# Optimization experiments

Hardware: AMD Instinct MI355X
Metric: run time of the kernel (lower is better)

## Reference

```python
import jax, jax.numpy as jnp
import numpy as np

DELTA_V = 0.5
DELTA_D = 1.5
ALPHA = 1.0
BETA = 1.0
GAMMA = 0.001
K = 32          # max number of instance labels per image
EPS = 1e-12     # sqrt safety for masked/degenerate distances


def setup_inputs() -> dict:
    key = jax.random.key(0)
    k1, k2 = jax.random.split(key)
    B, F, H, W = 8, 32, 512, 512
    embeds = jax.random.normal(k1, (B, F, H, W), dtype=jnp.float32)
    labels = jax.random.randint(k2, (B, 1, H, W), 0, K, dtype=jnp.int32)
    return {"embeds": embeds, "labels": labels}


def _disc_loss(embeds, labels):
    B, F, H, W = embeds.shape
    N = H * W
    x = embeds.reshape(B, F, N)                     # [B,F,N]
    lab = labels.reshape(B, N)                      # [B,N]

    oh = jax.nn.one_hot(lab, K, dtype=x.dtype)      # [B,N,K]
    counts = oh.sum(axis=1)                         # [B,K] pixels per label
    present = counts > 0                            # [B,K]
    pres_f = present.astype(x.dtype)
    C = pres_f.sum(axis=-1)                         # [B] number of instances
    safe_counts = jnp.maximum(counts, 1.0)

    # per-label means (fused segment reduction as one GEMM)
    sums = jnp.einsum('bfn,bnk->bfk', x, oh)        # [B,F,K]
    mu = sums / safe_counts[:, None, :]             # [B,F,K]

    # --- variance (pull) term ---
    mu_pix = jnp.einsum('bfk,bnk->bfn', mu, oh)     # mean broadcast back to pixels
    d = jnp.sqrt(jnp.sum((mu_pix - x) ** 2, axis=1) + EPS)   # [B,N] ||mu_c - x||
    v = jnp.maximum(d - DELTA_V, 0.0) ** 2
    v_per = jnp.einsum('bn,bnk->bk', v, oh) / safe_counts    # per-label mean
    var_b = jnp.where(C > 0, (v_per * pres_f).sum(-1) / jnp.maximum(C, 1.0), 0.0)
    var_loss = var_b.sum()

    # --- distance (push) term: pairwise between cluster means ---
    diff = mu[:, :, :, None] - mu[:, :, None, :]    # [B,F,K,K]
    dist = jnp.sqrt(jnp.sum(diff ** 2, axis=1) + EPS)        # [B,K,K]
    pair = present[:, :, None] & present[:, None, :]
    upper = jnp.triu(jnp.ones((K, K), dtype=bool), k=1)      # ca < cb pairs
    pm = pair & upper[None]
    hinge = jnp.maximum(DELTA_D - dist, 0.0) ** 2
    dloss = jnp.where(pm, hinge, 0.0).sum(axis=(-1, -2))     # [B]
    denom = jnp.maximum(C * (C - 1.0), 1.0)
    dis_loss = jnp.where(C > 2, dloss / denom, 0.0).sum()

    # --- regularization term: sum of ||mu_c|| over present labels ---
    mu_norm = jnp.sqrt(jnp.sum(mu ** 2, axis=1) + EPS)       # [B,K]
    reg_b = jnp.where(C > 1, (mu_norm * pres_f).sum(-1), 0.0)
    reg_loss = reg_b.sum()

    return ALPHA * var_loss + BETA * dis_loss + GAMMA * reg_loss


def reference(embeds, labels):
    return _disc_loss(embeds, labels)
```

## Files before the change

### kernel.cpp

```cpp
#include <hip/hip_runtime.h>

#define KLAB 32
#define FDIM 32
#define NPIX (512 * 512)
#define BATCH 8
#define EPSF 1e-12f

typedef __attribute__((ext_vector_type(8))) short bf16x8;
typedef __attribute__((ext_vector_type(4))) short bf16x4;
typedef __attribute__((ext_vector_type(4))) float f32x4;

__device__ __forceinline__ short f2bf(float f) {
    unsigned u = __builtin_bit_cast(unsigned, f);
    unsigned r = (u + 0x7FFFu + ((u >> 16) & 1u)) >> 16;
    return (short)r;
}

__device__ __forceinline__ float bf2f(short s) {
    return __builtin_bit_cast(float, (unsigned)((unsigned short)s) << 16);
}

__global__ __launch_bounds__(256) void k_msums(
    const float* __restrict__ x, const int* __restrict__ lab,
    float* __restrict__ g_sums, float* __restrict__ g_cnt,
    short* __restrict__ xbf)
{
    const int tid = threadIdx.x;
    const int b = blockIdx.y;
    const int w = tid >> 6, l = tid & 63;
    const int row = l & 15, grp = l >> 4;
    const int gw = blockIdx.x * 4 + w;
    const int STEPS = NPIX / 32 / 1024;
    const size_t xb = (size_t)b * FDIM * NPIX;
    const size_t lb = (size_t)b * NPIX;

    f32x4 acc00{}, acc01{}, acc10{}, acc11{}, accC0{}, accC1{};
    bf16x8 ones;
#pragma unroll
    for (int j = 0; j < 8; ++j) ones[j] = (short)0x3F80;

    const float* xr0 = x + xb + (size_t)row * NPIX;
    const float* xr1 = x + xb + (size_t)(row + 16) * NPIX;
    short* sr0 = xbf + xb + (size_t)row * NPIX;
    short* sr1 = xbf + xb + (size_t)(row + 16) * NPIX;

    int pg = gw * STEPS * 32 + grp * 8;
    int4 la = *reinterpret_cast<const int4*>(&lab[lb + pg]);
    int4 lc = *reinterpret_cast<const int4*>(&lab[lb + pg + 4]);
    f32x4 v0 = *reinterpret_cast<const f32x4*>(&xr0[pg]);
    f32x4 v1 = *reinterpret_cast<const f32x4*>(&xr0[pg + 4]);
    f32x4 v2 = *reinterpret_cast<const f32x4*>(&xr1[pg]);
    f32x4 v3 = *reinterpret_cast<const f32x4*>(&xr1[pg + 4]);

#pragma unroll 1
    for (int s = 0; s < STEPS; ++s) {
        const int pgn = pg + 32;
        int4 lan{}, lcn{};
        f32x4 w0{}, w1{}, w2{}, w3{};
        if (s + 1 < STEPS) {
            lan = *reinterpret_cast<const int4*>(&lab[lb + pgn]);
            lcn = *reinterpret_cast<const int4*>(&lab[lb + pgn + 4]);
            w0 = *reinterpret_cast<const f32x4*>(&xr0[pgn]);
            w1 = *reinterpret_cast<const f32x4*>(&xr0[pgn + 4]);
            w2 = *reinterpret_cast<const f32x4*>(&xr1[pgn]);
            w3 = *reinterpret_cast<const f32x4*>(&xr1[pgn + 4]);
        }

        bf16x8 a0, a1, b0, b1;
        a0[0]=f2bf(v0.x); a0[1]=f2bf(v0.y); a0[2]=f2bf(v0.z); a0[3]=f2bf(v0.w);
        a0[4]=f2bf(v1.x); a0[5]=f2bf(v1.y); a0[6]=f2bf(v1.z); a0[7]=f2bf(v1.w);
        a1[0]=f2bf(v2.x); a1[1]=f2bf(v2.y); a1[2]=f2bf(v2.z); a1[3]=f2bf(v2.w);
        a1[4]=f2bf(v3.x); a1[5]=f2bf(v3.y); a1[6]=f2bf(v3.z); a1[7]=f2bf(v3.w);
        const int lj[8] = {la.x, la.y, la.z, la.w, lc.x, lc.y, lc.z, lc.w};
#pragma unroll
        for (int j = 0; j < 8; ++j) {
            b0[j] = (lj[j] == row)      ? (short)0x3F80 : (short)0;
            b1[j] = (lj[j] == row + 16) ? (short)0x3F80 : (short)0;
        }

        *reinterpret_cast<bf16x8*>(&sr0[pg]) = a0;
        *reinterpret_cast<bf16x8*>(&sr1[pg]) = a1;

        acc00 = __builtin_amdgcn_mfma_f32_16x16x32_bf16(a0, b0, acc00, 0, 0, 0);
        acc10 = __builtin_amdgcn_mfma_f32_16x16x32_bf16(a1, b0, acc10, 0, 0, 0);
        acc01 = __builtin_amdgcn_mfma_f32_16x16x32_bf16(a0, b1, acc01, 0, 0, 0);
        acc11 = __builtin_amdgcn_mfma_f32_16x16x32_bf16(a1, b1, acc11, 0, 0, 0);
        accC0 = __builtin_amdgcn_mfma_f32_16x16x32_bf16(ones, b0, accC0, 0, 0, 0);
        accC1 = __builtin_amdgcn_mfma_f32_16x16x32_bf16(ones, b1, accC1, 0, 0, 0);

        la = lan; lc = lcn; v0 = w0; v1 = w1; v2 = w2; v3 = w3; pg = pgn;
    }

    __shared__ float s_red[4][FDIM * KLAB];
#pragma unroll
    for (int i = 0; i < 4; ++i) {
        const int fr = grp * 4 + i;
        s_red[w][(fr)      * KLAB + row]      = acc00[i];
        s_red[w][(fr)      * KLAB + row + 16] = acc01[i];
        s_red[w][(fr + 16) * KLAB + row]      = acc10[i];
        s_red[w][(fr + 16) * KLAB + row + 16] = acc11[i];
    }
    __syncthreads();
    float* gs = g_sums + (size_t)b * FDIM * KLAB;
    for (int i = tid; i < FDIM * KLAB; i += 256)
        atomicAdd(&gs[i], s_red[0][i] + s_red[1][i] + s_red[2][i] + s_red[3][i]);
    if (l < 16) {
        atomicAdd(&g_cnt[b * KLAB + l],      accC0[0]);
        atomicAdd(&g_cnt[b * KLAB + l + 16], accC1[0]);
    }
}

__global__ __launch_bounds__(256) void k_var(
    const short* __restrict__ xbf, const int* __restrict__ lab,
    const float* __restrict__ g_sums, const float* __restrict__ g_cnt,
    float* __restrict__ g_vsum)
{
    __shared__ float mu_s[FDIM][KLAB];
    __shared__ float vloc[KLAB];
    const int tid = threadIdx.x;
    const int b = blockIdx.y;
    for (int i = tid; i < FDIM * KLAB; i += 256) {
        const int k = i & (KLAB - 1);
        (&mu_s[0][0])[i] = g_sums[(size_t)b * FDIM * KLAB + i] / fmaxf(g_cnt[b * KLAB + k], 1.f);
    }
    if (tid < KLAB) vloc[tid] = 0.f;
    __syncthreads();

    const int n0 = blockIdx.x * 1024 + tid * 4;
    const size_t lb = (size_t)b * NPIX;
    const int4 l4 = *reinterpret_cast<const int4*>(&lab[lb + n0]);
    const int k0 = l4.x & 31, k1 = l4.y & 31, k2 = l4.z & 31, k3 = l4.w & 31;
    const short* xp = xbf + (size_t)b * FDIM * NPIX + n0;

    bf16x4 sl[4];
#pragma unroll
    for (int f = 0; f < 4; ++f)
        sl[f] = *reinterpret_cast<const bf16x4*>(xp + (size_t)f * NPIX);

    float d0 = 0.f, d1 = 0.f, d2 = 0.f, d3 = 0.f;
#pragma unroll
    for (int f = 0; f < FDIM; ++f) {
        const bf16x4 cur = sl[f & 3];
        if (f + 4 < FDIM)
            sl[f & 3] = *reinterpret_cast<const bf16x4*>(xp + (size_t)(f + 4) * NPIX);
        const float* mf = &mu_s[f][0];
        float t;
        t = bf2f(cur[0]) - mf[k0]; d0 += t * t;
        t = bf2f(cur[1]) - mf[k1]; d1 += t * t;
        t = bf2f(cur[2]) - mf[k2]; d2 += t * t;
        t = bf2f(cur[3]) - mf[k3]; d3 += t * t;
    }
    float h;
    h = fmaxf(sqrtf(d0 + EPSF) - 0.5f, 0.f); atomicAdd(&vloc[k0], h * h);
    h = fmaxf(sqrtf(d1 + EPSF) - 0.5f, 0.f); atomicAdd(&vloc[k1], h * h);
    h = fmaxf(sqrtf(d2 + EPSF) - 0.5f, 0.f); atomicAdd(&vloc[k2], h * h);
    h = fmaxf(sqrtf(d3 + EPSF) - 0.5f, 0.f); atomicAdd(&vloc[k3], h * h);
    __syncthreads();
    if (tid < KLAB) atomicAdd(&g_vsum[b * KLAB + tid], vloc[tid]);
}

__global__ __launch_bounds__(256) void k_final(
    const float* __restrict__ g_sums, const float* __restrict__ g_cnt,
    const float* __restrict__ g_vsum, float* __restrict__ out)
{
    __shared__ float mu8[BATCH][FDIM][KLAB];
    __shared__ float cnt8[BATCH][KLAB];
    __shared__ float tot[BATCH];
    const int tid = threadIdx.x;
    const int l = tid & 63, w = tid >> 6;

    for (int i = tid; i < BATCH * FDIM * KLAB; i += 256) {
        const int bb = i >> 10, k = i & 31;
        (&mu8[0][0][0])[i] = g_sums[i] / fmaxf(g_cnt[bb * KLAB + k], 1.f);
    }
    (&cnt8[0][0])[tid] = g_cnt[tid];
    __syncthreads();

    for (int half = 0; half < 2; ++half) {
        const int bb = w + half * 4;
        float pres = 0.f, varp = 0.f, regp = 0.f, distp = 0.f;
        if (l < KLAB && cnt8[bb][l] > 0.f) {
            pres = 1.f;
            varp = g_vsum[bb * KLAB + l] / fmaxf(cnt8[bb][l], 1.f);
            float s = 0.f;
            for (int f = 0; f < FDIM; ++f) { float m = mu8[bb][f][l]; s += m * m; }
            regp = sqrtf(s + EPSF);
        }
        for (int p = l; p < KLAB * KLAB; p += 64) {
            const int i = p >> 5, j = p & 31;
            if (i < j && cnt8[bb][i] > 0.f && cnt8[bb][j] > 0.f) {
                float s = 0.f;
                for (int f = 0; f < FDIM; ++f) {
                    float d = mu8[bb][f][i] - mu8[bb][f][j]; s += d * d;
                }
                const float dist = sqrtf(s + EPSF);
                const float hg = fmaxf(1.5f - dist, 0.f);
                distp += hg * hg;
            }
        }
        for (int m = 32; m > 0; m >>= 1) {
            pres  += __shfl_xor(pres,  m, 64);
            varp  += __shfl_xor(varp,  m, 64);
            regp  += __shfl_xor(regp,  m, 64);
            distp += __shfl_xor(distp, m, 64);
        }
        if (l == 0) {
            const float C = pres;
            const float var_b = (C > 0.f) ? varp / fmaxf(C, 1.f) : 0.f;
            const float dis_b = (C > 2.f) ? distp / fmaxf(C * (C - 1.f), 1.f) : 0.f;
            const float reg_b = (C > 1.f) ? regp : 0.f;
            tot[bb] = var_b + dis_b + 0.001f * reg_b;
        }
    }
    __syncthreads();
    if (tid == 0) {
        float t = 0.f;
        for (int bb = 0; bb < BATCH; ++bb) t += tot[bb];
        out[0] = t;
    }
}

extern "C" void kernel_launch(void* const* d_in, const int* in_sizes, int n_in,
                              void* d_out, int out_size, void* d_ws, size_t ws_size,
                              hipStream_t stream) {
    const float* x = (const float*)d_in[0];
    const int* lab = (const int*)d_in[1];
    float* out = (float*)d_out;

    const size_t XBF_BYTES = (size_t)BATCH * FDIM * NPIX * 2;
    short* xbf    = (short*)d_ws;
    float* g_sums = (float*)((char*)d_ws + XBF_BYTES);
    float* g_cnt  = g_sums + (size_t)BATCH * FDIM * KLAB;
    float* g_vsum = g_cnt + (size_t)BATCH * KLAB;
    hipMemsetAsync(g_sums, 0, (size_t)(BATCH * FDIM * KLAB + 2 * BATCH * KLAB) * 4, stream);

    dim3 grid1(256, BATCH);
    k_msums<<<grid1, 256, 0, stream>>>(x, lab, g_sums, g_cnt, xbf);
    dim3 grid2(256, BATCH);
    k_var<<<grid2, 256, 0, stream>>>(xbf, lab, g_sums, g_cnt, g_vsum);
    k_final<<<1, 256, 0, stream>>>(g_sums, g_cnt, g_vsum, out);
}
```

Baseline: 181.1 us.

## Stage bf16 embedding tiles through swizzled double-buffered LDS in mean-sum kernel

The segment-sum kernel no longer has each lane gather strided 8-element chunks from two feature rows. Each wave now loads 8 feature rows with fully coalesced float4 reads, converts them to bf16 and writes them both to the workspace and into an XOR-swizzled, double-buffered LDS tile. MFMA operands are then read back from LDS, with the next tile prefetched while the current one is consumed. The grid is halved and each block covers 2048 pixels, in exchange for a block barrier every iteration and extra LDS traffic.

```diff
diff --git a/kernel.cpp b/kernel.cpp
--- a/kernel.cpp
+++ b/kernel.cpp
@@ -20,90 +20,119 @@
     return __builtin_bit_cast(float, (unsigned)((unsigned short)s) << 16);
 }
 
-__global__ __launch_bounds__(256) void k_msums(
+__global__ __launch_bounds__(256, 4) void k_msums(
     const float* __restrict__ x, const int* __restrict__ lab,
     float* __restrict__ g_sums, float* __restrict__ g_cnt,
     short* __restrict__ xbf)
 {
+    __shared__ __align__(16) short alds[2][32 * 256];
+    __shared__ int lablds[2][256];
+
     const int tid = threadIdx.x;
     const int b = blockIdx.y;
+    const int cx = blockIdx.x;
     const int w = tid >> 6, l = tid & 63;
     const int row = l & 15, grp = l >> 4;
-    const int gw = blockIdx.x * 4 + w;
-    const int STEPS = NPIX / 32 / 1024;
     const size_t xb = (size_t)b * FDIM * NPIX;
     const size_t lb = (size_t)b * NPIX;
+    const int bp0 = cx * 2048;
+
+    const float* xw = x + xb + (size_t)(w * 8) * NPIX;
+    short* xbw = xbf + xb + (size_t)(w * 8) * NPIX;
 
     f32x4 acc00{}, acc01{}, acc10{}, acc11{}, accC0{}, accC1{};
     bf16x8 ones;
 #pragma unroll
     for (int j = 0; j < 8; ++j) ones[j] = (short)0x3F80;
 
-    const float* xr0 = x + xb + (size_t)row * NPIX;
-    const float* xr1 = x + xb + (size_t)(row + 16) * NPIX;
-    short* sr0 = xbf + xb + (size_t)row * NPIX;
-    short* sr1 = xbf + xb + (size_t)(row + 16) * NPIX;
-
-    int pg = gw * STEPS * 32 + grp * 8;
-    int4 la = *reinterpret_cast<const int4*>(&lab[lb + pg]);
-    int4 lc = *reinterpret_cast<const int4*>(&lab[lb + pg + 4]);
-    f32x4 v0 = *reinterpret_cast<const f32x4*>(&xr0[pg]);
-    f32x4 v1 = *reinterpret_cast<const f32x4*>(&xr0[pg + 4]);
-    f32x4 v2 = *reinterpret_cast<const f32x4*>(&xr1[pg]);
-    f32x4 v3 = *reinterpret_cast<const f32x4*>(&xr1[pg + 4]);
+    f32x4 sv[8];
+    int slab;
+
+    {
+        const int sp = bp0;
+#pragma unroll
+        for (int r = 0; r < 8; ++r)
+            sv[r] = *reinterpret_cast<const f32x4*>(xw + (size_t)r * NPIX + sp + l * 4);
+        slab = lab[lb + sp + tid];
+#pragma unroll
+        for (int r = 0; r < 8; ++r) {
+            bf16x4 c;
+            c[0]=f2bf(sv[r].x); c[1]=f2bf(sv[r].y); c[2]=f2bf(sv[r].z); c[3]=f2bf(sv[r].w);
+            *reinterpret_cast<bf16x4*>(xbw + (size_t)r * NPIX + sp + l * 4) = c;
+            const int f = w * 8 + r;
+            *reinterpret_cast<bf16x4*>((char*)&alds[0][0] + ((f * 512 + l * 8) ^ (r << 4))) = c;
+        }
+        lablds[0][tid] = slab;
+    }
+    __syncthreads();
 
 #pragma unroll 1
-    for (int s = 0; s < STEPS; ++s) {
-        const int pgn = pg + 32;
-        int4 lan{}, lcn{};
-        f32x4 w0{}, w1{}, w2{}, w3{};
-        if (s + 1 < STEPS) {
-            lan = *reinterpret_cast<const int4*>(&lab[lb + pgn]);
-            lcn = *reinterpret_cast<const int4*>(&lab[lb + pgn + 4]);
-            w0 = *reinterpret_cast<const f32x4*>(&xr0[pgn]);
-            w1 = *reinterpret_cast<const f32x4*>(&xr0[pgn + 4]);
-            w2 = *reinterpret_cast<const f32x4*>(&xr1[pgn]);
-            w3 = *reinterpret_cast<const f32x4*>(&xr1[pgn + 4]);
-        }
-
-        bf16x8 a0, a1, b0, b1;
-        a0[0]=f2bf(v0.x); a0[1]=f2bf(v0.y); a0[2]=f2bf(v0.z); a0[3]=f2bf(v0.w);
-        a0[4]=f2bf(v1.x); a0[5]=f2bf(v1.y); a0[6]=f2bf(v1.z); a0[7]=f2bf(v1.w);
-        a1[0]=f2bf(v2.x); a1[1]=f2bf(v2.y); a1[2]=f2bf(v2.z); a1[3]=f2bf(v2.w);
-        a1[4]=f2bf(v3.x); a1[5]=f2bf(v3.y); a1[6]=f2bf(v3.z); a1[7]=f2bf(v3.w);
-        const int lj[8] = {la.x, la.y, la.z, la.w, lc.x, lc.y, lc.z, lc.w};
-#pragma unroll
-        for (int j = 0; j < 8; ++j) {
-            b0[j] = (lj[j] == row)      ? (short)0x3F80 : (short)0;
-            b1[j] = (lj[j] == row + 16) ? (short)0x3F80 : (short)0;
-        }
-
-        *reinterpret_cast<bf16x8*>(&sr0[pg]) = a0;
-        *reinterpret_cast<bf16x8*>(&sr1[pg]) = a1;
-
-        acc00 = __builtin_amdgcn_mfma_f32_16x16x32_bf16(a0, b0, acc00, 0, 0, 0);
-        acc10 = __builtin_amdgcn_mfma_f32_16x16x32_bf16(a1, b0, acc10, 0, 0, 0);
-        acc01 = __builtin_amdgcn_mfma_f32_16x16x32_bf16(a0, b1, acc01, 0, 0, 0);
-        acc11 = __builtin_amdgcn_mfma_f32_16x16x32_bf16(a1, b1, acc11, 0, 0, 0);
-        accC0 = __builtin_amdgcn_mfma_f32_16x16x32_bf16(ones, b0, accC0, 0, 0, 0);
-        accC1 = __builtin_amdgcn_mfma_f32_16x16x32_bf16(ones, b1, accC1, 0, 0, 0);
-
-        la = lan; lc = lcn; v0 = w0; v1 = w1; v2 = w2; v3 = w3; pg = pgn;
-    }
-
-    __shared__ float s_red[4][FDIM * KLAB];
+    for (int t = 0; t < 8; ++t) {
+        const int cb = t & 1, nb = cb ^ 1;
+
+        if (t + 1 < 8) {
+            const int sp = bp0 + (t + 1) * 256;
+#pragma unroll
+            for (int r = 0; r < 8; ++r)
+                sv[r] = *reinterpret_cast<const f32x4*>(xw + (size_t)r * NPIX + sp + l * 4);
+            slab = lab[lb + sp + tid];
+        }
+
+#pragma unroll
+        for (int kq = 0; kq < 2; ++kq) {
+            const int kk = 2 * w + kq;
+            const int cbyte = (kk * 32 + grp * 8) * 2;
+            const int swz = (row & 7) << 4;
+            const bf16x8 a0 = *reinterpret_cast<const bf16x8*>(
+                (char*)&alds[cb][0] + ((row * 512 + cbyte) ^ swz));
+            const bf16x8 a1 = *reinterpret_cast<const bf16x8*>(
+                (char*)&alds[cb][0] + (((row + 16) * 512 + cbyte) ^ swz));
+            const int base = kk * 32 + grp * 8;
+            const int4 la = *reinterpret_cast<const int4*>(&lablds[cb][base]);
+            const int4 lc = *reinterpret_cast<const int4*>(&lablds[cb][base + 4]);
+            bf16x8 b0, b1;
+            const int lj[8] = {la.x, la.y, la.z, la.w, lc.x, lc.y, lc.z, lc.w};
+#pragma unroll
+            for (int j = 0; j < 8; ++j) {
+                b0[j] = (lj[j] == row)      ? (short)0x3F80 : (short)0;
+                b1[j] = (lj[j] == row + 16) ? (short)0x3F80 : (short)0;
+            }
+            acc00 = __builtin_amdgcn_mfma_f32_16x16x32_bf16(a0, b0, acc00, 0, 0, 0);
+            acc10 = __builtin_amdgcn_mfma_f32_16x16x32_bf16(a1, b0, acc10, 0, 0, 0);
+            acc01 = __builtin_amdgcn_mfma_f32_16x16x32_bf16(a0, b1, acc01, 0, 0, 0);
+            acc11 = __builtin_amdgcn_mfma_f32_16x16x32_bf16(a1, b1, acc11, 0, 0, 0);
+            accC0 = __builtin_amdgcn_mfma_f32_16x16x32_bf16(ones, b0, accC0, 0, 0, 0);
+            accC1 = __builtin_amdgcn_mfma_f32_16x16x32_bf16(ones, b1, accC1, 0, 0, 0);
+        }
+
+        if (t + 1 < 8) {
+            const int sp = bp0 + (t + 1) * 256;
+#pragma unroll
+            for (int r = 0; r < 8; ++r) {
+                bf16x4 c;
+                c[0]=f2bf(sv[r].x); c[1]=f2bf(sv[r].y); c[2]=f2bf(sv[r].z); c[3]=f2bf(sv[r].w);
+                *reinterpret_cast<bf16x4*>(xbw + (size_t)r * NPIX + sp + l * 4) = c;
+                const int f = w * 8 + r;
+                *reinterpret_cast<bf16x4*>((char*)&alds[nb][0] + ((f * 512 + l * 8) ^ (r << 4))) = c;
+            }
+            lablds[nb][tid] = slab;
+        }
+        __syncthreads();
+    }
+
+    float* s_red = reinterpret_cast<float*>(&alds[0][0]);
 #pragma unroll
     for (int i = 0; i < 4; ++i) {
         const int fr = grp * 4 + i;
-        s_red[w][(fr)      * KLAB + row]      = acc00[i];
-        s_red[w][(fr)      * KLAB + row + 16] = acc01[i];
-        s_red[w][(fr + 16) * KLAB + row]      = acc10[i];
-        s_red[w][(fr + 16) * KLAB + row + 16] = acc11[i];
+        s_red[w * 1024 + (fr)      * KLAB + row]      = acc00[i];
+        s_red[w * 1024 + (fr)      * KLAB + row + 16] = acc01[i];
+        s_red[w * 1024 + (fr + 16) * KLAB + row]      = acc10[i];
+        s_red[w * 1024 + (fr + 16) * KLAB + row + 16] = acc11[i];
     }
     __syncthreads();
     float* gs = g_sums + (size_t)b * FDIM * KLAB;
     for (int i = tid; i < FDIM * KLAB; i += 256)
-        atomicAdd(&gs[i], s_red[0][i] + s_red[1][i] + s_red[2][i] + s_red[3][i]);
+        atomicAdd(&gs[i], s_red[i] + s_red[1024 + i] + s_red[2048 + i] + s_red[3072 + i]);
     if (l < 16) {
         atomicAdd(&g_cnt[b * KLAB + l],      accC0[0]);
         atomicAdd(&g_cnt[b * KLAB + l + 16], accC1[0]);
@@ -234,7 +263,7 @@
     float* g_vsum = g_cnt + (size_t)BATCH * KLAB;
     hipMemsetAsync(g_sums, 0, (size_t)(BATCH * FDIM * KLAB + 2 * BATCH * KLAB) * 4, stream);
 
-    dim3 grid1(256, BATCH);
+    dim3 grid1(128, BATCH);
     k_msums<<<grid1, 256, 0, stream>>>(x, lab, g_sums, g_cnt, xbf);
     dim3 grid2(256, BATCH);
     k_var<<<grid2, 256, 0, stream>>>(xbf, lab, g_sums, g_cnt, g_vsum);
```

Result: faster. 148.7 us (-17.9%).

## Split bf16 conversion and label packing into a separate streaming kernel

Applied to the files above, without the earlier changes.

Adds a grid-stride kernel that converts the fp32 embeddings to bf16 and packs the int32 labels into bytes. The segment-sum kernel then reads bf16 data and byte labels through a four-deep unrolled prefetch ring, and the variance kernel reads packed labels. The aim is to shrink label traffic in both passes and give the MFMA pass a simpler load pattern. The cost is an extra kernel launch and a full extra read of the bf16 buffer in the sums pass, which was previously fused with the conversion.

```diff
diff --git a/kernel.cpp b/kernel.cpp
--- a/kernel.cpp
+++ b/kernel.cpp
@@ -20,17 +20,40 @@
     return __builtin_bit_cast(float, (unsigned)((unsigned short)s) << 16);
 }
 
+__global__ __launch_bounds__(256) void k_cvt(
+    const float* __restrict__ x, const int* __restrict__ lab,
+    short* __restrict__ xbf, unsigned char* __restrict__ labp)
+{
+    const int tid = blockIdx.x * 256 + threadIdx.x;
+    const int nthr = gridDim.x * 256;
+    const int nx8 = BATCH * FDIM * NPIX / 8;
+    for (int i = tid; i < nx8; i += nthr) {
+        const size_t o = (size_t)i * 8;
+        const f32x4 v0 = *reinterpret_cast<const f32x4*>(&x[o]);
+        const f32x4 v1 = *reinterpret_cast<const f32x4*>(&x[o + 4]);
+        bf16x8 c;
+        c[0]=f2bf(v0.x); c[1]=f2bf(v0.y); c[2]=f2bf(v0.z); c[3]=f2bf(v0.w);
+        c[4]=f2bf(v1.x); c[5]=f2bf(v1.y); c[6]=f2bf(v1.z); c[7]=f2bf(v1.w);
+        *reinterpret_cast<bf16x8*>(&xbf[o]) = c;
+    }
+    const int nl4 = BATCH * NPIX / 4;
+    for (int i = tid; i < nl4; i += nthr) {
+        const int4 l4 = *reinterpret_cast<const int4*>(&lab[(size_t)i * 4]);
+        const unsigned p = (unsigned)(l4.x & 255) | ((unsigned)(l4.y & 255) << 8) |
+                           ((unsigned)(l4.z & 255) << 16) | ((unsigned)(l4.w & 255) << 24);
+        *reinterpret_cast<unsigned*>(&labp[(size_t)i * 4]) = p;
+    }
+}
+
 __global__ __launch_bounds__(256) void k_msums(
-    const float* __restrict__ x, const int* __restrict__ lab,
-    float* __restrict__ g_sums, float* __restrict__ g_cnt,
-    short* __restrict__ xbf)
+    const short* __restrict__ xbf, const unsigned char* __restrict__ labp,
+    float* __restrict__ g_sums, float* __restrict__ g_cnt)
 {
     const int tid = threadIdx.x;
     const int b = blockIdx.y;
     const int w = tid >> 6, l = tid & 63;
     const int row = l & 15, grp = l >> 4;
     const int gw = blockIdx.x * 4 + w;
-    const int STEPS = NPIX / 32 / 1024;
     const size_t xb = (size_t)b * FDIM * NPIX;
     const size_t lb = (size_t)b * NPIX;
 
@@ -39,57 +62,43 @@
 #pragma unroll
     for (int j = 0; j < 8; ++j) ones[j] = (short)0x3F80;
 
-    const float* xr0 = x + xb + (size_t)row * NPIX;
-    const float* xr1 = x + xb + (size_t)(row + 16) * NPIX;
-    short* sr0 = xbf + xb + (size_t)row * NPIX;
-    short* sr1 = xbf + xb + (size_t)(row + 16) * NPIX;
-
-    int pg = gw * STEPS * 32 + grp * 8;
-    int4 la = *reinterpret_cast<const int4*>(&lab[lb + pg]);
-    int4 lc = *reinterpret_cast<const int4*>(&lab[lb + pg + 4]);
-    f32x4 v0 = *reinterpret_cast<const f32x4*>(&xr0[pg]);
-    f32x4 v1 = *reinterpret_cast<const f32x4*>(&xr0[pg + 4]);
-    f32x4 v2 = *reinterpret_cast<const f32x4*>(&xr1[pg]);
-    f32x4 v3 = *reinterpret_cast<const f32x4*>(&xr1[pg + 4]);
-
-#pragma unroll 1
-    for (int s = 0; s < STEPS; ++s) {
-        const int pgn = pg + 32;
-        int4 lan{}, lcn{};
-        f32x4 w0{}, w1{}, w2{}, w3{};
-        if (s + 1 < STEPS) {
-            lan = *reinterpret_cast<const int4*>(&lab[lb + pgn]);
-            lcn = *reinterpret_cast<const int4*>(&lab[lb + pgn + 4]);
-            w0 = *reinterpret_cast<const f32x4*>(&xr0[pgn]);
-            w1 = *reinterpret_cast<const f32x4*>(&xr0[pgn + 4]);
-            w2 = *reinterpret_cast<const f32x4*>(&xr1[pgn]);
-            w3 = *reinterpret_cast<const f32x4*>(&xr1[pgn + 4]);
-        }
-
-        bf16x8 a0, a1, b0, b1;
-        a0[0]=f2bf(v0.x); a0[1]=f2bf(v0.y); a0[2]=f2bf(v0.z); a0[3]=f2bf(v0.w);
-        a0[4]=f2bf(v1.x); a0[5]=f2bf(v1.y); a0[6]=f2bf(v1.z); a0[7]=f2bf(v1.w);
-        a1[0]=f2bf(v2.x); a1[1]=f2bf(v2.y); a1[2]=f2bf(v2.z); a1[3]=f2bf(v2.w);
-        a1[4]=f2bf(v3.x); a1[5]=f2bf(v3.y); a1[6]=f2bf(v3.z); a1[7]=f2bf(v3.w);
-        const int lj[8] = {la.x, la.y, la.z, la.w, lc.x, lc.y, lc.z, lc.w};
+    const short* xr0 = xbf + xb + (size_t)row * NPIX;
+    const short* xr1 = xbf + xb + (size_t)(row + 16) * NPIX;
+
+    bf16x8 sa0[4], sa1[4];
+    unsigned long long slb[4];
+
+#define LOADG(s, slot) do {                                                   \
+    const int pg = (gw * 8 + (s)) * 32 + grp * 8;                             \
+    sa0[slot] = *reinterpret_cast<const bf16x8*>(&xr0[pg]);                   \
+    sa1[slot] = *reinterpret_cast<const bf16x8*>(&xr1[pg]);                   \
+    slb[slot] = *reinterpret_cast<const unsigned long long*>(&labp[lb + pg]); \
+    __builtin_amdgcn_sched_barrier(0);     \
+    } while (0)
+
+    LOADG(0, 0); LOADG(1, 1); LOADG(2, 2); LOADG(3, 3);
+
+#pragma unroll
+    for (int s = 0; s < 8; ++s) {
+        const bf16x8 a0 = sa0[s & 3];
+        const bf16x8 a1 = sa1[s & 3];
+        const unsigned long long L = slb[s & 3];
+        if (s + 4 < 8) LOADG(s + 4, s & 3);
+        bf16x8 b0, b1;
 #pragma unroll
         for (int j = 0; j < 8; ++j) {
-            b0[j] = (lj[j] == row)      ? (short)0x3F80 : (short)0;
-            b1[j] = (lj[j] == row + 16) ? (short)0x3F80 : (short)0;
-        }
-
-        *reinterpret_cast<bf16x8*>(&sr0[pg]) = a0;
-        *reinterpret_cast<bf16x8*>(&sr1[pg]) = a1;
-
+            const int lj = (int)((L >> (8 * j)) & 0xFF);
+            b0[j] = (lj == row)      ? (short)0x3F80 : (short)0;
+            b1[j] = (lj == row + 16) ? (short)0x3F80 : (short)0;
+        }
         acc00 = __builtin_amdgcn_mfma_f32_16x16x32_bf16(a0, b0, acc00, 0, 0, 0);
         acc10 = __builtin_amdgcn_mfma_f32_16x16x32_bf16(a1, b0, acc10, 0, 0, 0);
         acc01 = __builtin_amdgcn_mfma_f32_16x16x32_bf16(a0, b1, acc01, 0, 0, 0);
         acc11 = __builtin_amdgcn_mfma_f32_16x16x32_bf16(a1, b1, acc11, 0, 0, 0);
         accC0 = __builtin_amdgcn_mfma_f32_16x16x32_bf16(ones, b0, accC0, 0, 0, 0);
         accC1 = __builtin_amdgcn_mfma_f32_16x16x32_bf16(ones, b1, accC1, 0, 0, 0);
-
-        la = lan; lc = lcn; v0 = w0; v1 = w1; v2 = w2; v3 = w3; pg = pgn;
-    }
+    }
+#undef LOADG
 
     __shared__ float s_red[4][FDIM * KLAB];
 #pragma unroll
@@ -111,7 +120,7 @@
 }
 
 __global__ __launch_bounds__(256) void k_var(
-    const short* __restrict__ xbf, const int* __restrict__ lab,
+    const short* __restrict__ xbf, const unsigned char* __restrict__ labp,
     const float* __restrict__ g_sums, const float* __restrict__ g_cnt,
     float* __restrict__ g_vsum)
 {
@@ -128,8 +137,8 @@
 
     const int n0 = blockIdx.x * 1024 + tid * 4;
     const size_t lb = (size_t)b * NPIX;
-    const int4 l4 = *reinterpret_cast<const int4*>(&lab[lb + n0]);
-    const int k0 = l4.x & 31, k1 = l4.y & 31, k2 = l4.z & 31, k3 = l4.w & 31;
+    const unsigned lp = *reinterpret_cast<const unsigned*>(&labp[lb + n0]);
+    const int k0 = lp & 0xFF, k1 = (lp >> 8) & 0xFF, k2 = (lp >> 16) & 0xFF, k3 = lp >> 24;
     const short* xp = xbf + (size_t)b * FDIM * NPIX + n0;
 
     bf16x4 sl[4];
@@ -228,15 +237,18 @@
     float* out = (float*)d_out;
 
     const size_t XBF_BYTES = (size_t)BATCH * FDIM * NPIX * 2;
+    const size_t LABP_BYTES = (size_t)BATCH * NPIX;
     short* xbf    = (short*)d_ws;
-    float* g_sums = (float*)((char*)d_ws + XBF_BYTES);
+    unsigned char* labp = (unsigned char*)d_ws + XBF_BYTES;
+    float* g_sums = (float*)((char*)d_ws + XBF_BYTES + LABP_BYTES);
     float* g_cnt  = g_sums + (size_t)BATCH * FDIM * KLAB;
     float* g_vsum = g_cnt + (size_t)BATCH * KLAB;
     hipMemsetAsync(g_sums, 0, (size_t)(BATCH * FDIM * KLAB + 2 * BATCH * KLAB) * 4, stream);
 
+    k_cvt<<<2048, 256, 0, stream>>>(x, lab, xbf, labp);
     dim3 grid1(256, BATCH);
-    k_msums<<<grid1, 256, 0, stream>>>(x, lab, g_sums, g_cnt, xbf);
+    k_msums<<<grid1, 256, 0, stream>>>(xbf, labp, g_sums, g_cnt);
     dim3 grid2(256, BATCH);
-    k_var<<<grid2, 256, 0, stream>>>(xbf, lab, g_sums, g_cnt, g_vsum);
+    k_var<<<grid2, 256, 0, stream>>>(xbf, labp, g_sums, g_cnt, g_vsum);
     k_final<<<1, 256, 0, stream>>>(g_sums, g_cnt, g_vsum, out);
 }
```

New measurement: 196.9 us. +8.7%, slower.
